# Kernel optimization log

Hardware: AMD Instinct MI355X
Metric: run time of the kernel (lower is better)

The kernel has to match this reference:

```python
import jax, jax.numpy as jnp
import numpy as np

B, N, D, H = 2, 256, 512, 8
DK = D // H


def _lin(x, w, b):
    # torch nn.Linear: y = x @ W.T + b, W is [out, in]
    return jnp.matmul(x, w.T) + b


def setup_inputs() -> dict:
    key = jax.random.key(0)
    ks = jax.random.split(key, 12)
    std = 0.02
    inp = {
        "x": jax.random.normal(ks[0], (B, N, D), jnp.float32),
        "batched_graphs": jax.random.normal(ks[1], (B, N, N, D), jnp.float32) * std,
        "mask": jnp.zeros((B, N, N), dtype=bool),
    }
    names = ["wq", "wk", "wv", "wo", "wl", "wr", "wrk", "wrv"]
    for i, n in enumerate(names):
        inp[n] = jax.random.normal(ks[2 + i], (D, D), jnp.float32) * std
        inp["b" + n[1:]] = jnp.zeros((D,), jnp.float32)
    return inp


def reference(x, batched_graphs, mask,
              wq, bq, wk, bk, wv, bv, wo, bo,
              wl, bl, wr, br, wrk, brk, wrv, brv):
    # update_relations: per-edge key/value maps
    graphs_k = _lin(batched_graphs, wrk, brk).reshape(B, N, N, H, DK)
    graphs_v = _lin(batched_graphs, wrv, brv).reshape(B, N, N, H, DK)

    query = _lin(x, wq, bq).reshape(B, N, H, DK)
    key_ = _lin(x, wk, bk).reshape(B, N, H, DK)
    value = _lin(x, wv, bv).reshape(B, N, H, DK)

    scores_k = jnp.einsum("bxhd,byhd->bxyh", query, key_)
    scores_g = jnp.einsum("bxhd,bxyhd->bxyh", query, graphs_k)
    scores = (scores_k + scores_g) / np.sqrt(DK).astype(np.float32)
    scores = jnp.where(mask[..., None], jnp.float32(-1e9), scores)
    p_attn = jax.nn.softmax(scores, axis=2)  # over key nodes y

    x_v = jnp.einsum("bxyh,byhd->bxhd", p_attn, value)
    x_g = jnp.einsum("bxyh,bxyhd->bxhd", p_attn, graphs_v)
    out = (x_v + x_g).reshape(B, N, D)

    # relation update: outer sum of left/right projections
    x_left = _lin(out, wl, bl)[:, :, None, :]   # [B,N,1,D]
    x_right = _lin(out, wr, br)[:, None, :, :]  # [B,1,N,D]
    new_graphs = x_left + x_right               # [B,N,N,D]

    return _lin(out, wo, bo), new_graphs
```

## Files before the change

### kernel.cpp

```cpp
#include <hip/hip_runtime.h>

#define BB 2
#define NN 256
#define DD 512
#define HH 8

typedef float f4raw __attribute__((ext_vector_type(4)));

__device__ __forceinline__ float dot4(float4 a, float4 b) {
    return a.x*b.x + a.y*b.y + a.z*b.z + a.w*b.w;
}

__device__ __forceinline__ float4 f4fma(float s, float4 a, float4 acc) {
    acc.x += s * a.x; acc.y += s * a.y; acc.z += s * a.z; acc.w += s * a.w;
    return acc;
}

__device__ __forceinline__ void gload_lds16(const void* g, void* l) {
    __builtin_amdgcn_global_load_lds(
        (const __attribute__((address_space(1))) unsigned int*)g,
        (__attribute__((address_space(3))) unsigned int*)l, 16, 0, 0);
}

__device__ __forceinline__ void stage_swz8(const char* rowbase, float4* dst, int w, int lane) {
    #pragma unroll
    for (int j = 0; j < 2; ++j) {
        const int f0 = w * 128 + j * 64;
        const int y = w;
        const int c = j * 64 + lane;
        gload_lds16(rowbase + (size_t)y * 2048 + ((size_t)(c ^ y) << 4), &dst[f0]);
    }
}

__global__ __launch_bounds__(64) void kProj(
    const float* __restrict__ in_,
    const float* __restrict__ w0, const float* __restrict__ b0,
    const float* __restrict__ w1, const float* __restrict__ b1,
    const float* __restrict__ w2, const float* __restrict__ b2,
    float* __restrict__ o0, float* __restrict__ o1, float* __restrict__ o2)
{
    __shared__ float4 xs[2][32 * 5];
    __shared__ float4 ws[2][32 * 5];

    const int t = threadIdx.x;
    const int blk = blockIdx.x;
    const int proj = blk >> 8;
    const int rem = blk & 255;
    const int row0 = (rem >> 4) * 32;
    const int col0 = (rem & 15) * 32;

    const float* W; const float* Bp; float* O;
    if (proj == 0)      { W = w0; Bp = b0; O = o0; }
    else if (proj == 1) { W = w1; Bp = b1; O = o1; }
    else                { W = w2; Bp = b2; O = o2; }

    const float4* X4 = (const float4*)in_ + (size_t)row0 * 128;
    const float4* W4 = (const float4*)W  + (size_t)col0 * 128;

    const int sr = t >> 2, se = t & 3;
    const int ty = t >> 3, tx = t & 7;

    float4 rx0 = X4[(size_t)sr * 128 + se];
    float4 rx1 = X4[(size_t)(sr + 16) * 128 + se];
    float4 rw0 = W4[(size_t)sr * 128 + se];
    float4 rw1 = W4[(size_t)(sr + 16) * 128 + se];
    xs[0][sr * 5 + se] = rx0;  xs[0][(sr + 16) * 5 + se] = rx1;
    ws[0][sr * 5 + se] = rw0;  ws[0][(sr + 16) * 5 + se] = rw1;

    float acc[4][4] = {};

    for (int q = 0; q < 32; ++q) {
        __syncthreads();
        const int cur = q & 1;
        if (q < 31) {
            const int ko = (q + 1) * 4;
            rx0 = X4[(size_t)sr * 128 + ko + se];
            rx1 = X4[(size_t)(sr + 16) * 128 + ko + se];
            rw0 = W4[(size_t)sr * 128 + ko + se];
            rw1 = W4[(size_t)(sr + 16) * 128 + ko + se];
        }
        const float4* xb = xs[cur];
        const float4* wb = ws[cur];
        #pragma unroll
        for (int e4 = 0; e4 < 4; ++e4) {
            float4 xr[4], wc[4];
            #pragma unroll
            for (int i = 0; i < 4; ++i) xr[i] = xb[(ty + 8 * i) * 5 + e4];
            #pragma unroll
            for (int j = 0; j < 4; ++j) wc[j] = wb[(tx + 8 * j) * 5 + e4];
            #pragma unroll
            for (int i = 0; i < 4; ++i)
                #pragma unroll
                for (int j = 0; j < 4; ++j)
                    acc[i][j] += dot4(xr[i], wc[j]);
        }
        if (q < 31) {
            const int nxt = cur ^ 1;
            xs[nxt][sr * 5 + se] = rx0;  xs[nxt][(sr + 16) * 5 + se] = rx1;
            ws[nxt][sr * 5 + se] = rw0;  ws[nxt][(sr + 16) * 5 + se] = rw1;
        }
    }

    float bb[4];
    #pragma unroll
    for (int j = 0; j < 4; ++j) bb[j] = Bp[col0 + tx + 8 * j];
    #pragma unroll
    for (int i = 0; i < 4; ++i) {
        const int orow = row0 + ty + 8 * i;
        #pragma unroll
        for (int j = 0; j < 4; ++j)
            O[(size_t)orow * DD + col0 + tx + 8 * j] = acc[i][j] + bb[j];
    }
}

__global__ __launch_bounds__(256) void kQkp(
    const float* __restrict__ q, const float* __restrict__ wrk,
    float* __restrict__ qkp)
{
    __shared__ float qs[8 * 64];
    const int t = threadIdx.x;
    const int blk = blockIdx.x;
    const int rowg = blk >> 5;
    const int h = (blk >> 2) & 7;
    const int eq = blk & 3;
    const int row0 = rowg * 8;
    {
        const int r = t >> 5, d2 = (t & 31) * 2;
        const float2 tmp = *(const float2*)(q + (size_t)(row0 + r) * DD + h * 64 + d2);
        qs[r * 64 + d2] = tmp.x; qs[r * 64 + d2 + 1] = tmp.y;
    }
    __syncthreads();
    const int e = eq * 128 + (t & 127);
    const int rp = (t >> 7) * 4;
    const float* wcol = wrk + (size_t)(h * 64) * DD + e;
    float a0 = 0, a1 = 0, a2 = 0, a3 = 0;
    #pragma unroll 8
    for (int d = 0; d < 64; ++d) {
        const float wv = wcol[(size_t)d * DD];
        a0 += qs[(rp + 0) * 64 + d] * wv;
        a1 += qs[(rp + 1) * 64 + d] * wv;
        a2 += qs[(rp + 2) * 64 + d] * wv;
        a3 += qs[(rp + 3) * 64 + d] * wv;
    }
    qkp[((size_t)(row0 + rp + 0) * HH + h) * DD + e] = a0;
    qkp[((size_t)(row0 + rp + 1) * HH + h) * DD + e] = a1;
    qkp[((size_t)(row0 + rp + 2) * HH + h) * DD + e] = a2;
    qkp[((size_t)(row0 + rp + 3) * HH + h) * DD + e] = a3;
}

__global__ __launch_bounds__(256) void kSk(
    const float* __restrict__ q, const float* __restrict__ k,
    const unsigned char* __restrict__ mask, float* __restrict__ sk)
{
    __shared__ float qs[8 * 65];
    __shared__ float ks[64 * 65];
    const int t = threadIdx.x;
    const int blk = blockIdx.x;
    const int b  = blk >> 10;
    const int h  = (blk >> 7) & 7;
    const int xt = (blk >> 2) & 31;
    const int yt = blk & 3;
    const int x0 = xt * 8, y0 = yt * 64;
    {
        const int r = t >> 5, d2 = (t & 31) * 2;
        const float2 tmp = *(const float2*)(q + (size_t)(b * NN + x0 + r) * DD + h * 64 + d2);
        qs[r * 65 + d2] = tmp.x; qs[r * 65 + d2 + 1] = tmp.y;
    }
    #pragma unroll
    for (int j = 0; j < 8; ++j) {
        const int f = t + 256 * j;
        const int r = f >> 5, d2 = (f & 31) * 2;
        const float2 tmp = *(const float2*)(k + (size_t)(b * NN + y0 + r) * DD + h * 64 + d2);
        ks[r * 65 + d2] = tmp.x; ks[r * 65 + d2 + 1] = tmp.y;
    }
    __syncthreads();
    const int xi = t >> 5, yg = t & 31;
    float a0 = 0, a1 = 0;
    #pragma unroll 8
    for (int d = 0; d < 64; ++d) {
        const float qv = qs[xi * 65 + d];
        a0 += qv * ks[(yg * 2 + 0) * 65 + d];
        a1 += qv * ks[(yg * 2 + 1) * 65 + d];
    }
    a0 *= 0.125f; a1 *= 0.125f;
    const unsigned char* mrow = mask + (size_t)(b * NN + x0 + xi) * NN;
    const int gy = y0 + yg * 2;
    if (mrow[gy + 0]) a0 = -1e9f;
    if (mrow[gy + 1]) a1 = -1e9f;
    float2 st; st.x = a0; st.y = a1;
    *(float2*)(sk + ((size_t)(b * NN + x0 + xi) * HH + h) * NN + gy) = st;
}

__global__ __launch_bounds__(512) void kC(
    const float* __restrict__ G, const float* __restrict__ sk,
    const float* __restrict__ qkp, const float* __restrict__ v,
    const float* __restrict__ wrv, const float* __restrict__ brv,
    float* __restrict__ om)
{
    __shared__ float4 gbuf[2][1024];
    __shared__ float4 qgc[1024];
    __shared__ float s_l[64];
    __shared__ float lL[8];
    __shared__ float xvs[512];

    const int t = threadIdx.x;
    const int lane = t & 63;
    const int w = t >> 6;
    const int bid = blockIdx.x;
    const int b = bid >> 8;

    const char* Grow = (const char*)(G + (size_t)bid * NN * DD);
    stage_swz8((const char*)(qkp + (size_t)bid * HH * DD), qgc, w, lane);
    stage_swz8(Grow, &gbuf[0][0], w, lane);

    const int s_  = t & 15;
    const int sg  = t >> 4;
    const int sy  = sg >> 2;
    const int h0i = (sg & 3) * 2;
    const int ec4 = t & 127;
    const int hb  = (t >> 7) * 2;
    const int hv  = t >> 6;
    const int dv  = t & 63;
    const int ri  = hv & 1;

    float4 gacc0 = {0,0,0,0}, gacc1 = {0,0,0,0};
    float m0 = -3e38f, m1 = -3e38f, l0 = 0, l1 = 0, vx = 0;

    const float* vcol = v + (size_t)(b * NN) * DD + hv * 64 + dv;
    const float* skrow = sk + (size_t)bid * HH * NN;

    __syncthreads();

    int cb = 0;
    for (int tt = 0; tt < 32; ++tt) {
        if (tt < 31)
            stage_swz8(Grow + (size_t)(tt + 1) * 8 * 2048, &gbuf[cb ^ 1][0], w, lane);

        float vvs[8];
        #pragma unroll
        for (int y = 0; y < 8; ++y) vvs[y] = vcol[((size_t)tt * 8 + y) * DD];

        {
            float a0 = 0, a1 = 0;
            const float4* gb = &gbuf[cb][0];
            #pragma unroll
            for (int i = 0; i < 8; ++i) {
                const int e4 = i * 16 + s_;
                const float4 g0 = gb[sy * 128 + (e4 ^ sy)];
                a0 += dot4(g0, qgc[h0i * 128 + (e4 ^ h0i)]);
                a1 += dot4(g0, qgc[(h0i + 1) * 128 + (e4 ^ (h0i + 1))]);
            }
            #pragma unroll
            for (int mm = 1; mm < 16; mm <<= 1) {
                a0 += __shfl_xor(a0, mm); a1 += __shfl_xor(a1, mm);
            }
            if (s_ < 2) {
                const float val = (s_ == 0) ? a0 : a1;
                const int h = h0i + s_;
                const int gy = tt * 8 + sy;
                s_l[sy * 8 + h] = val * 0.125f + skrow[(size_t)h * NN + gy];
            }
        }
        __syncthreads();

        float2 sv[8];
        #pragma unroll
        for (int y = 0; y < 8; ++y) sv[y] = *(const float2*)&s_l[y * 8 + hb];

        float mx0 = sv[0].x, mx1 = sv[0].y;
        #pragma unroll
        for (int y = 1; y < 8; ++y) {
            mx0 = fmaxf(mx0, sv[y].x); mx1 = fmaxf(mx1, sv[y].y);
        }
        const float n0 = fmaxf(m0, mx0), rs0 = __expf(m0 - n0);
        const float n1 = fmaxf(m1, mx1), rs1 = __expf(m1 - n1);
        m0 = n0; m1 = n1;
        l0 *= rs0; l1 *= rs1;
        gacc0.x *= rs0; gacc0.y *= rs0; gacc0.z *= rs0; gacc0.w *= rs0;
        gacc1.x *= rs1; gacc1.y *= rs1; gacc1.z *= rs1; gacc1.w *= rs1;
        vx *= ri ? rs1 : rs0;

        {
            const float4* gb = &gbuf[cb][0];
            #pragma unroll
            for (int y = 0; y < 8; ++y) {
                const float4 gv = gb[y * 128 + (ec4 ^ y)];
                const float p0 = __expf(sv[y].x - m0); l0 += p0; gacc0 = f4fma(p0, gv, gacc0);
                const float p1 = __expf(sv[y].y - m1); l1 += p1; gacc1 = f4fma(p1, gv, gacc1);
                vx += (ri ? p1 : p0) * vvs[y];
            }
        }
        __syncthreads();
        cb ^= 1;
    }

    qgc[(hb + 0) * 128 + ec4] = gacc0;
    qgc[(hb + 1) * 128 + ec4] = gacc1;
    if (ec4 == 0) { lL[hb] = l0; lL[hb + 1] = l1; }
    xvs[hv * 64 + dv] = vx;
    __syncthreads();

    #pragma unroll 2
    for (int oo = 0; oo < 16; ++oo) {
        const int o = sg * 16 + oo;
        const int ho = o >> 6;
        const float4* wr4 = (const float4*)(wrv + (size_t)o * DD);
        float acc = 0;
        #pragma unroll
        for (int i = 0; i < 8; ++i) {
            const int e4 = i * 16 + s_;
            acc += dot4(wr4[e4], qgc[ho * 128 + e4]);
        }
        #pragma unroll
        for (int mm = 1; mm < 16; mm <<= 1) acc += __shfl_xor(acc, mm);
        if (s_ == 0)
            om[(size_t)bid * DD + o] = (xvs[o] + acc) / lL[ho] + brv[o];
    }
}

__global__ __launch_bounds__(256) void kE(
    const float* __restrict__ xl, const float* __restrict__ xr,
    float* __restrict__ ng)
{
    const int t = threadIdx.x;
    const int blk = blockIdx.x;
    const int bid = blk >> 2;
    const int yc = blk & 3;
    const int b = bid >> 8;
    const int o4 = t & 127;
    const int yh = t >> 7;
    const float4 left = ((const float4*)xl)[(size_t)bid * 128 + o4];
    const float4* xr4 = (const float4*)xr + (size_t)b * NN * 128;
    f4raw* out4 = (f4raw*)ng + (size_t)bid * NN * 128;
    for (int y = yc * 64 + yh; y < yc * 64 + 64; y += 2) {
        const float4 rr = xr4[y * 128 + o4];
        f4raw s;
        s.x = left.x + rr.x; s.y = left.y + rr.y;
        s.z = left.z + rr.z; s.w = left.w + rr.w;
        __builtin_nontemporal_store(s, &out4[y * 128 + o4]);
    }
}

extern "C" void kernel_launch(void* const* d_in, const int* in_sizes, int n_in,
                              void* d_out, int out_size, void* d_ws, size_t ws_size,
                              hipStream_t stream)
{
    (void)in_sizes; (void)n_in; (void)out_size; (void)ws_size;
    const float* x    = (const float*)d_in[0];
    const float* G    = (const float*)d_in[1];
    const unsigned char* mask = (const unsigned char*)d_in[2];
    const float* wq  = (const float*)d_in[3];  const float* bq  = (const float*)d_in[4];
    const float* wk  = (const float*)d_in[5];  const float* bk  = (const float*)d_in[6];
    const float* wv  = (const float*)d_in[7];  const float* bv  = (const float*)d_in[8];
    const float* wo  = (const float*)d_in[9];  const float* bo  = (const float*)d_in[10];
    const float* wl  = (const float*)d_in[11]; const float* bl  = (const float*)d_in[12];
    const float* wr  = (const float*)d_in[13]; const float* br  = (const float*)d_in[14];
    const float* wrk = (const float*)d_in[15];
    const float* wrv = (const float*)d_in[17]; const float* brv = (const float*)d_in[18];

    float* out  = (float*)d_out;
    float* fout = out;
    float* ng   = out + (size_t)BB * NN * DD;

    const size_t ng_f  = (size_t)BB * NN * NN * DD;
    const size_t row_f = (size_t)BB * NN * DD;
    const size_t total = row_f * 17;
    float* base = ng + ng_f - total;
    float* q    = base;
    float* k    = q   + row_f;
    float* vv_  = k   + row_f;
    float* qkp  = vv_ + row_f;
    float* skp  = qkp + row_f * 8;
    float* om   = skp + row_f * 4;
    float* xl = (float*)d_ws;
    float* xr = xl + row_f;

    kProj<<<768, 64, 0, stream>>>(x, wq, bq, wk, bk, wv, bv, q, k, vv_);
    kQkp <<<2048, 256, 0, stream>>>(q, wrk, qkp);
    kSk  <<<2048, 256, 0, stream>>>(q, k, mask, skp);
    kC   <<<512, 512, 0, stream>>>(G, skp, qkp, vv_, wrv, brv, om);
    kProj<<<768, 64, 0, stream>>>(om, wo, bo, wl, bl, wr, br, fout, xl, xr);
    kE   <<<2048, 256, 0, stream>>>(xl, xr, ng);
}
```

Measured before the change: 305.7 us.

## Restructure edge-attention kernel into per-wave independent online softmax with split reduction

The main attention kernel moves from 512 to 256 threads. Each wave now owns two key rows per tile and keeps its own online-softmax state for all eight heads, so the per-tile block barriers go away and only explicit vmcnt waits gate the double-buffered global-to-LDS loads of G. The per-wave partial results are merged with a log-sum-exp combine and an LDS tree reduction. The value-side term is computed afterwards from stored scores instead of inside the loop. This trades more registers per thread and a serial 256-step value loop at the end for fewer synchronizations and better occupancy.

```diff
diff --git a/kernel.cpp b/kernel.cpp
--- a/kernel.cpp
+++ b/kernel.cpp
@@ -16,19 +16,36 @@
     return acc;
 }
 
+__device__ __forceinline__ float4 f4mul(float s, float4 a) {
+    a.x *= s; a.y *= s; a.z *= s; a.w *= s; return a;
+}
+
 __device__ __forceinline__ void gload_lds16(const void* g, void* l) {
     __builtin_amdgcn_global_load_lds(
         (const __attribute__((address_space(1))) unsigned int*)g,
         (__attribute__((address_space(3))) unsigned int*)l, 16, 0, 0);
 }
 
-__device__ __forceinline__ void stage_swz8(const char* rowbase, float4* dst, int w, int lane) {
-    #pragma unroll
-    for (int j = 0; j < 2; ++j) {
-        const int f0 = w * 128 + j * 64;
-        const int y = w;
-        const int c = j * 64 + lane;
+__device__ __forceinline__ void stage_swz(const char* rowbase, float4* dst, int w, int lane) {
+    #pragma unroll
+    for (int j = 0; j < 4; ++j) {
+        const int f0 = w * 256 + j * 64;
+        const int y = f0 >> 7;
+        const int c = (f0 & 127) + lane;
         gload_lds16(rowbase + (size_t)y * 2048 + ((size_t)(c ^ y) << 4), &dst[f0]);
+    }
+}
+
+__device__ __forceinline__ void stageG(const char* Grow, int tt, int w, int lane, float4* dst) {
+    #pragma unroll
+    for (int r = 0; r < 2; ++r) {
+        const int yr = 2 * w + r;
+        const char* src = Grow + (size_t)(tt * 8 + yr) * 2048;
+        #pragma unroll
+        for (int j = 0; j < 2; ++j) {
+            const int c = j * 64 + lane;
+            gload_lds16(src + ((size_t)(c ^ yr) << 4), &dst[r * 128 + j * 64]);
+        }
     }
 }
 
@@ -191,17 +208,17 @@
     *(float2*)(sk + ((size_t)(b * NN + x0 + xi) * HH + h) * NN + gy) = st;
 }
 
-__global__ __launch_bounds__(512) void kC(
+__global__ __launch_bounds__(256, 2) void kC(
     const float* __restrict__ G, const float* __restrict__ sk,
     const float* __restrict__ qkp, const float* __restrict__ v,
     const float* __restrict__ wrv, const float* __restrict__ brv,
     float* __restrict__ om)
 {
-    __shared__ float4 gbuf[2][1024];
-    __shared__ float4 qgc[1024];
-    __shared__ float s_l[64];
-    __shared__ float lL[8];
-    __shared__ float xvs[512];
+    __shared__ float4 Gdb[2][4][256];
+    __shared__ float4 qk4[1024];
+    __shared__ float  sk_l[2048];
+    __shared__ float  s_st[2048];
+    __shared__ float  ml[64];
 
     const int t = threadIdx.x;
     const int lane = t & 63;
@@ -210,111 +227,185 @@
     const int b = bid >> 8;
 
     const char* Grow = (const char*)(G + (size_t)bid * NN * DD);
-    stage_swz8((const char*)(qkp + (size_t)bid * HH * DD), qgc, w, lane);
-    stage_swz8(Grow, &gbuf[0][0], w, lane);
-
-    const int s_  = t & 15;
-    const int sg  = t >> 4;
-    const int sy  = sg >> 2;
-    const int h0i = (sg & 3) * 2;
-    const int ec4 = t & 127;
-    const int hb  = (t >> 7) * 2;
-    const int hv  = t >> 6;
-    const int dv  = t & 63;
-    const int ri  = hv & 1;
-
-    float4 gacc0 = {0,0,0,0}, gacc1 = {0,0,0,0};
-    float m0 = -3e38f, m1 = -3e38f, l0 = 0, l1 = 0, vx = 0;
-
-    const float* vcol = v + (size_t)(b * NN) * DD + hv * 64 + dv;
-    const float* skrow = sk + (size_t)bid * HH * NN;
-
-    __syncthreads();
+
+    stage_swz((const char*)(qkp + (size_t)bid * HH * DD), qk4, w, lane);
+    {
+        const char* skb = (const char*)(sk + (size_t)bid * HH * NN);
+        gload_lds16(skb + (size_t)(w * 128 + lane) * 16,      (float4*)sk_l + w * 128);
+        gload_lds16(skb + (size_t)(w * 128 + 64 + lane) * 16, (float4*)sk_l + w * 128 + 64);
+    }
+    stageG(Grow, 0, w, lane, &Gdb[0][w][0]);
+    asm volatile("s_waitcnt vmcnt(4)" ::: "memory");
+    __builtin_amdgcn_sched_barrier(0);
+    __builtin_amdgcn_s_barrier();
+
+    const int s_ = lane & 15;
+    const int g  = lane >> 4;
+    const int h0 = 2 * g;
+    const int yr0 = 2 * w, yr1 = 2 * w + 1;
+
+    float4 gA[8], gB[8];
+    float m[8], l[8];
+    #pragma unroll
+    for (int h = 0; h < 8; ++h) {
+        gA[h] = make_float4(0, 0, 0, 0); gB[h] = make_float4(0, 0, 0, 0);
+        m[h] = -3e38f; l[h] = 0.f;
+    }
 
     int cb = 0;
+    #pragma unroll 1
     for (int tt = 0; tt < 32; ++tt) {
-        if (tt < 31)
-            stage_swz8(Grow + (size_t)(tt + 1) * 8 * 2048, &gbuf[cb ^ 1][0], w, lane);
-
-        float vvs[8];
-        #pragma unroll
-        for (int y = 0; y < 8; ++y) vvs[y] = vcol[((size_t)tt * 8 + y) * DD];
+        __builtin_amdgcn_sched_barrier(0);
+        if (tt < 31) {
+            stageG(Grow, tt + 1, w, lane, &Gdb[cb ^ 1][w][0]);
+            asm volatile("s_waitcnt vmcnt(4)" ::: "memory");
+        } else {
+            asm volatile("s_waitcnt vmcnt(0)" ::: "memory");
+        }
+        __builtin_amdgcn_sched_barrier(0);
+
+        const float4* gb = &Gdb[cb][w][0];
+        const int gy0 = tt * 8 + yr0, gy1 = tt * 8 + yr1;
 
         {
-            float a0 = 0, a1 = 0;
-            const float4* gb = &gbuf[cb][0];
+            float a00 = 0, a01 = 0, a10 = 0, a11 = 0;
             #pragma unroll
             for (int i = 0; i < 8; ++i) {
                 const int e4 = i * 16 + s_;
-                const float4 g0 = gb[sy * 128 + (e4 ^ sy)];
-                a0 += dot4(g0, qgc[h0i * 128 + (e4 ^ h0i)]);
-                a1 += dot4(g0, qgc[(h0i + 1) * 128 + (e4 ^ (h0i + 1))]);
+                const float4 g0 = gb[(e4 ^ yr0)];
+                const float4 g1 = gb[128 + (e4 ^ yr1)];
+                const float4 p0 = qk4[h0 * 128 + (e4 ^ h0)];
+                const float4 p1 = qk4[(h0 + 1) * 128 + (e4 ^ (h0 + 1))];
+                a00 += dot4(g0, p0); a01 += dot4(g0, p1);
+                a10 += dot4(g1, p0); a11 += dot4(g1, p1);
             }
             #pragma unroll
             for (int mm = 1; mm < 16; mm <<= 1) {
-                a0 += __shfl_xor(a0, mm); a1 += __shfl_xor(a1, mm);
+                a00 += __shfl_xor(a00, mm); a01 += __shfl_xor(a01, mm);
+                a10 += __shfl_xor(a10, mm); a11 += __shfl_xor(a11, mm);
             }
-            if (s_ < 2) {
-                const float val = (s_ == 0) ? a0 : a1;
-                const int h = h0i + s_;
-                const int gy = tt * 8 + sy;
-                s_l[sy * 8 + h] = val * 0.125f + skrow[(size_t)h * NN + gy];
+            if (s_ < 4) {
+                const int yy = s_ & 1, hh = s_ >> 1;
+                const float val = yy ? (hh ? a11 : a10) : (hh ? a01 : a00);
+                const int h = h0 + hh;
+                const int gy = yy ? gy1 : gy0;
+                s_st[gy * 8 + h] = val * 0.125f + sk_l[h * 256 + gy];
             }
         }
-        __syncthreads();
-
-        float2 sv[8];
-        #pragma unroll
-        for (int y = 0; y < 8; ++y) sv[y] = *(const float2*)&s_l[y * 8 + hb];
-
-        float mx0 = sv[0].x, mx1 = sv[0].y;
-        #pragma unroll
-        for (int y = 1; y < 8; ++y) {
-            mx0 = fmaxf(mx0, sv[y].x); mx1 = fmaxf(mx1, sv[y].y);
-        }
-        const float n0 = fmaxf(m0, mx0), rs0 = __expf(m0 - n0);
-        const float n1 = fmaxf(m1, mx1), rs1 = __expf(m1 - n1);
-        m0 = n0; m1 = n1;
-        l0 *= rs0; l1 *= rs1;
-        gacc0.x *= rs0; gacc0.y *= rs0; gacc0.z *= rs0; gacc0.w *= rs0;
-        gacc1.x *= rs1; gacc1.y *= rs1; gacc1.z *= rs1; gacc1.w *= rs1;
-        vx *= ri ? rs1 : rs0;
-
-        {
-            const float4* gb = &gbuf[cb][0];
-            #pragma unroll
-            for (int y = 0; y < 8; ++y) {
-                const float4 gv = gb[y * 128 + (ec4 ^ y)];
-                const float p0 = __expf(sv[y].x - m0); l0 += p0; gacc0 = f4fma(p0, gv, gacc0);
-                const float p1 = __expf(sv[y].y - m1); l1 += p1; gacc1 = f4fma(p1, gv, gacc1);
-                vx += (ri ? p1 : p0) * vvs[y];
-            }
-        }
-        __syncthreads();
+
+        const float4 sva = *(const float4*)&s_st[gy0 * 8];
+        const float4 svb = *(const float4*)&s_st[gy0 * 8 + 4];
+        const float4 svc = *(const float4*)&s_st[gy1 * 8];
+        const float4 svd = *(const float4*)&s_st[gy1 * 8 + 4];
+        const float s0[8] = {sva.x, sva.y, sva.z, sva.w, svb.x, svb.y, svb.z, svb.w};
+        const float s1[8] = {svc.x, svc.y, svc.z, svc.w, svd.x, svd.y, svd.z, svd.w};
+
+        const float4 gr0a = gb[(lane ^ yr0)];
+        const float4 gr0b = gb[((lane + 64) ^ yr0)];
+        const float4 gr1a = gb[128 + (lane ^ yr1)];
+        const float4 gr1b = gb[128 + ((lane + 64) ^ yr1)];
+
+        #pragma unroll
+        for (int h = 0; h < 8; ++h) {
+            const float mn = fmaxf(m[h], fmaxf(s0[h], s1[h]));
+            const float rs = __expf(m[h] - mn);
+            const float p0 = __expf(s0[h] - mn);
+            const float p1 = __expf(s1[h] - mn);
+            m[h] = mn;
+            l[h] = l[h] * rs + p0 + p1;
+            gA[h] = f4fma(p1, gr1a, f4fma(p0, gr0a, f4mul(rs, gA[h])));
+            gB[h] = f4fma(p1, gr1b, f4fma(p0, gr0b, f4mul(rs, gB[h])));
+        }
         cb ^= 1;
     }
 
-    qgc[(hb + 0) * 128 + ec4] = gacc0;
-    qgc[(hb + 1) * 128 + ec4] = gacc1;
-    if (ec4 == 0) { lL[hb] = l0; lL[hb + 1] = l1; }
-    xvs[hv * 64 + dv] = vx;
-    __syncthreads();
-
-    #pragma unroll 2
-    for (int oo = 0; oo < 16; ++oo) {
-        const int o = sg * 16 + oo;
-        const int ho = o >> 6;
+    asm volatile("s_waitcnt vmcnt(0)" ::: "memory");
+    __syncthreads();
+    if (lane == 0) {
+        #pragma unroll
+        for (int h = 0; h < 8; ++h) { ml[w * 16 + h] = m[h]; ml[w * 16 + 8 + h] = l[h]; }
+    }
+    __syncthreads();
+
+    float M[8], Lf[8];
+    #pragma unroll
+    for (int h = 0; h < 8; ++h) {
+        const float m0 = ml[h], m1 = ml[16 + h], m2 = ml[32 + h], m3 = ml[48 + h];
+        const float mm = fmaxf(fmaxf(m0, m1), fmaxf(m2, m3));
+        M[h] = mm;
+        Lf[h] = __expf(m0 - mm) * ml[8 + h]  + __expf(m1 - mm) * ml[24 + h]
+              + __expf(m2 - mm) * ml[40 + h] + __expf(m3 - mm) * ml[56 + h];
+    }
+    #pragma unroll
+    for (int h = 0; h < 8; ++h) {
+        const float ws = __expf(m[h] - M[h]);
+        gA[h] = f4mul(ws, gA[h]); gB[h] = f4mul(ws, gB[h]);
+    }
+    float4* rA = &Gdb[0][0][0];
+    float4* rB = &Gdb[1][0][0];
+    if (w == 2) {
+        #pragma unroll
+        for (int h = 0; h < 8; ++h) { rA[h * 128 + lane] = gA[h]; rA[h * 128 + 64 + lane] = gB[h]; }
+    }
+    if (w == 3) {
+        #pragma unroll
+        for (int h = 0; h < 8; ++h) { rB[h * 128 + lane] = gA[h]; rB[h * 128 + 64 + lane] = gB[h]; }
+    }
+    __syncthreads();
+    if (w == 0) {
+        #pragma unroll
+        for (int h = 0; h < 8; ++h) {
+            gA[h].x += rA[h*128+lane].x; gA[h].y += rA[h*128+lane].y; gA[h].z += rA[h*128+lane].z; gA[h].w += rA[h*128+lane].w;
+            gB[h].x += rA[h*128+64+lane].x; gB[h].y += rA[h*128+64+lane].y; gB[h].z += rA[h*128+64+lane].z; gB[h].w += rA[h*128+64+lane].w;
+        }
+    }
+    if (w == 1) {
+        #pragma unroll
+        for (int h = 0; h < 8; ++h) {
+            gA[h].x += rB[h*128+lane].x; gA[h].y += rB[h*128+lane].y; gA[h].z += rB[h*128+lane].z; gA[h].w += rB[h*128+lane].w;
+            gB[h].x += rB[h*128+64+lane].x; gB[h].y += rB[h*128+64+lane].y; gB[h].z += rB[h*128+64+lane].z; gB[h].w += rB[h*128+64+lane].w;
+        }
+    }
+    __syncthreads();
+    if (w == 1) {
+        #pragma unroll
+        for (int h = 0; h < 8; ++h) { rA[h * 128 + lane] = gA[h]; rA[h * 128 + 64 + lane] = gB[h]; }
+    }
+    __syncthreads();
+    if (w == 0) {
+        #pragma unroll
+        for (int h = 0; h < 8; ++h) {
+            gA[h].x += rA[h*128+lane].x; gA[h].y += rA[h*128+lane].y; gA[h].z += rA[h*128+lane].z; gA[h].w += rA[h*128+lane].w;
+            gB[h].x += rA[h*128+64+lane].x; gB[h].y += rA[h*128+64+lane].y; gB[h].z += rA[h*128+64+lane].z; gB[h].w += rA[h*128+64+lane].w;
+            qk4[h * 128 + lane] = gA[h];
+            qk4[h * 128 + 64 + lane] = gB[h];
+        }
+    }
+    if (t == 0) {
+        #pragma unroll
+        for (int h = 0; h < 8; ++h) ml[h] = Lf[h];
+    }
+    {
+        #pragma unroll
+        for (int h = 0; h < 8; ++h) sk_l[t * 8 + h] = __expf(s_st[t * 8 + h] - M[h]);
+    }
+    __syncthreads();
+
+    const float* vb = v + (size_t)(b * NN) * DD;
+    #pragma unroll
+    for (int jj = 0; jj < 2; ++jj) {
+        const int o = jj * 256 + t;
+        const int h = o >> 6, d = o & 63;
         const float4* wr4 = (const float4*)(wrv + (size_t)o * DD);
+        const float4* gf = (const float4*)qk4 + h * 128;
         float acc = 0;
-        #pragma unroll
-        for (int i = 0; i < 8; ++i) {
-            const int e4 = i * 16 + s_;
-            acc += dot4(wr4[e4], qgc[ho * 128 + e4]);
-        }
-        #pragma unroll
-        for (int mm = 1; mm < 16; mm <<= 1) acc += __shfl_xor(acc, mm);
-        if (s_ == 0)
-            om[(size_t)bid * DD + o] = (xvs[o] + acc) / lL[ho] + brv[o];
+        #pragma unroll 4
+        for (int e4 = 0; e4 < 128; ++e4) acc += dot4(wr4[e4], gf[e4]);
+        float xv = 0;
+        const float* vc = vb + h * 64 + d;
+        #pragma unroll 4
+        for (int y = 0; y < 256; ++y) xv += sk_l[y * 8 + h] * vc[(size_t)y * DD];
+        om[(size_t)bid * DD + o] = (xv + acc) / ml[h] + brv[o];
     }
 }
 
@@ -364,7 +455,7 @@
 
     const size_t ng_f  = (size_t)BB * NN * NN * DD;
     const size_t row_f = (size_t)BB * NN * DD;
-    const size_t total = row_f * 17;
+    const size_t total = row_f * 16;
     float* base = ng + ng_f - total;
     float* q    = base;
     float* k    = q   + row_f;
@@ -378,7 +469,7 @@
     kProj<<<768, 64, 0, stream>>>(x, wq, bq, wk, bk, wv, bv, q, k, vv_);
     kQkp <<<2048, 256, 0, stream>>>(q, wrk, qkp);
     kSk  <<<2048, 256, 0, stream>>>(q, k, mask, skp);
-    kC   <<<512, 512, 0, stream>>>(G, skp, qkp, vv_, wrv, brv, om);
+    kC   <<<512, 256, 0, stream>>>(G, skp, qkp, vv_, wrv, brv, om);
     kProj<<<768, 64, 0, stream>>>(om, wo, bo, wl, bl, wr, br, fout, xl, xr);
     kE   <<<2048, 256, 0, stream>>>(xl, xr, ng);
 }
```

Measured after the change: 291.4 us. 1.05x faster.

## Split attention over key ranges into partial blocks with separate merge kernel

Applied to the files above, without the earlier changes.

The main attention kernel now splits each query row's 256 keys into four parts across 2048 blocks of 256 threads. Each block reads G directly into registers rather than staging it through LDS, and runs an online softmax per wave, merging the waves through LDS. Partial max, sum and accumulators go to scratch memory, and a new merge kernel combines them and applies the wrv projection. The aim is more parallelism and occupancy on the G stream, which dominates memory traffic, at the cost of an extra launch and partial-result traffic.

```diff
diff --git a/kernel.cpp b/kernel.cpp
--- a/kernel.cpp
+++ b/kernel.cpp
@@ -16,18 +16,22 @@
     return acc;
 }
 
+__device__ __forceinline__ float4 f4mul(float s, float4 a) {
+    a.x *= s; a.y *= s; a.z *= s; a.w *= s; return a;
+}
+
 __device__ __forceinline__ void gload_lds16(const void* g, void* l) {
     __builtin_amdgcn_global_load_lds(
         (const __attribute__((address_space(1))) unsigned int*)g,
         (__attribute__((address_space(3))) unsigned int*)l, 16, 0, 0);
 }
 
-__device__ __forceinline__ void stage_swz8(const char* rowbase, float4* dst, int w, int lane) {
-    #pragma unroll
-    for (int j = 0; j < 2; ++j) {
-        const int f0 = w * 128 + j * 64;
-        const int y = w;
-        const int c = j * 64 + lane;
+__device__ __forceinline__ void stage_swz(const char* rowbase, float4* dst, int w, int lane) {
+    #pragma unroll
+    for (int j = 0; j < 4; ++j) {
+        const int f0 = w * 256 + j * 64;
+        const int y = f0 >> 7;
+        const int c = (f0 & 127) + lane;
         gload_lds16(rowbase + (size_t)y * 2048 + ((size_t)(c ^ y) << 4), &dst[f0]);
     }
 }
@@ -191,131 +195,236 @@
     *(float2*)(sk + ((size_t)(b * NN + x0 + xi) * HH + h) * NN + gy) = st;
 }
 
-__global__ __launch_bounds__(512) void kC(
+__global__ __launch_bounds__(256, 3) void kC(
     const float* __restrict__ G, const float* __restrict__ sk,
     const float* __restrict__ qkp, const float* __restrict__ v,
+    float* __restrict__ pg, float* __restrict__ pxv,
+    float* __restrict__ pm, float* __restrict__ pl)
+{
+    __shared__ float4 qk4[1024];
+    __shared__ float4 mrg[1024];
+    __shared__ float4 xvm[128];
+    __shared__ float  ml[64];
+
+    const int t = threadIdx.x;
+    const int lane = t & 63;
+    const int w = t >> 6;
+    const int blk = blockIdx.x;
+    const int part = blk & 3;
+    const int bid = blk >> 2;
+    const int b = bid >> 8;
+    const int ybase = part * 64;
+
+    const int s_ = lane & 15;
+    const int g  = lane >> 4;
+    const int h0 = 2 * g, h1 = 2 * g + 1;
+    const int yr0 = 2 * w, yr1 = 2 * w + 1;
+
+    stage_swz((const char*)(qkp + (size_t)bid * HH * DD), qk4, w, lane);
+    asm volatile("s_waitcnt vmcnt(0)" ::: "memory");
+    __syncthreads();
+
+    float4 gagg0[8], gagg1[8];
+    #pragma unroll
+    for (int i = 0; i < 8; ++i) {
+        gagg0[i] = make_float4(0, 0, 0, 0);
+        gagg1[i] = make_float4(0, 0, 0, 0);
+    }
+    float4 xv0 = {0, 0, 0, 0}, xv1 = {0, 0, 0, 0};
+    float m0 = -3e38f, m1 = -3e38f, l0 = 0.f, l1 = 0.f;
+
+    const float4* Gb  = (const float4*)(G + (size_t)bid * NN * DD);
+    const float*  skb = sk + (size_t)bid * HH * NN;
+    const float4* vb4 = (const float4*)(v + (size_t)(b * NN) * DD);
+
+    #pragma unroll 1
+    for (int tt = 0; tt < 8; ++tt) {
+        const int gy0 = ybase + tt * 8 + yr0;
+        const int gy1 = gy0 + 1;
+
+        const float sk00 = skb[h0 * NN + gy0], sk01 = skb[h1 * NN + gy0];
+        const float sk10 = skb[h0 * NN + gy1], sk11 = skb[h1 * NN + gy1];
+        const float4 v00 = vb4[(size_t)gy0 * 128 + h0 * 16 + s_];
+        const float4 v01 = vb4[(size_t)gy0 * 128 + h1 * 16 + s_];
+        const float4 v10 = vb4[(size_t)gy1 * 128 + h0 * 16 + s_];
+        const float4 v11 = vb4[(size_t)gy1 * 128 + h1 * 16 + s_];
+
+        float4 g0[8], g1[8];
+        #pragma unroll
+        for (int i = 0; i < 8; ++i) g0[i] = Gb[(size_t)gy0 * 128 + i * 16 + s_];
+        #pragma unroll
+        for (int i = 0; i < 8; ++i) g1[i] = Gb[(size_t)gy1 * 128 + i * 16 + s_];
+
+        float a00 = 0, a01 = 0, a10 = 0, a11 = 0;
+        #pragma unroll
+        for (int i = 0; i < 8; ++i) {
+            const int e4 = i * 16 + s_;
+            const float4 q0 = qk4[h0 * 128 + (e4 ^ h0)];
+            const float4 q1 = qk4[h1 * 128 + (e4 ^ h1)];
+            a00 += dot4(g0[i], q0); a01 += dot4(g0[i], q1);
+            a10 += dot4(g1[i], q0); a11 += dot4(g1[i], q1);
+        }
+        #pragma unroll
+        for (int mm = 1; mm < 16; mm <<= 1) {
+            a00 += __shfl_xor(a00, mm); a01 += __shfl_xor(a01, mm);
+            a10 += __shfl_xor(a10, mm); a11 += __shfl_xor(a11, mm);
+        }
+        const float s00 = a00 * 0.125f + sk00;
+        const float s01 = a01 * 0.125f + sk01;
+        const float s10 = a10 * 0.125f + sk10;
+        const float s11 = a11 * 0.125f + sk11;
+
+        const float mn0 = fmaxf(m0, fmaxf(s00, s10));
+        const float rs0 = __expf(m0 - mn0);
+        const float p00 = __expf(s00 - mn0), p10 = __expf(s10 - mn0);
+        m0 = mn0; l0 = l0 * rs0 + p00 + p10;
+        const float mn1 = fmaxf(m1, fmaxf(s01, s11));
+        const float rs1 = __expf(m1 - mn1);
+        const float p01 = __expf(s01 - mn1), p11 = __expf(s11 - mn1);
+        m1 = mn1; l1 = l1 * rs1 + p01 + p11;
+
+        #pragma unroll
+        for (int i = 0; i < 8; ++i) {
+            gagg0[i] = f4fma(p10, g1[i], f4fma(p00, g0[i], f4mul(rs0, gagg0[i])));
+            gagg1[i] = f4fma(p11, g1[i], f4fma(p01, g0[i], f4mul(rs1, gagg1[i])));
+        }
+        xv0 = f4fma(p10, v10, f4fma(p00, v00, f4mul(rs0, xv0)));
+        xv1 = f4fma(p11, v11, f4fma(p01, v01, f4mul(rs1, xv1)));
+    }
+
+    if (s_ == 0) {
+        ml[w * 16 + h0] = m0;      ml[w * 16 + h1] = m1;
+        ml[w * 16 + 8 + h0] = l0;  ml[w * 16 + 8 + h1] = l1;
+    }
+    __syncthreads();
+    float M0, M1, L0, L1;
+    {
+        const float q0 = ml[h0], q1 = ml[16 + h0], q2 = ml[32 + h0], q3 = ml[48 + h0];
+        M0 = fmaxf(fmaxf(q0, q1), fmaxf(q2, q3));
+        L0 = __expf(q0 - M0) * ml[8 + h0]  + __expf(q1 - M0) * ml[24 + h0]
+           + __expf(q2 - M0) * ml[40 + h0] + __expf(q3 - M0) * ml[56 + h0];
+        const float r0 = ml[h1], r1 = ml[16 + h1], r2 = ml[32 + h1], r3 = ml[48 + h1];
+        M1 = fmaxf(fmaxf(r0, r1), fmaxf(r2, r3));
+        L1 = __expf(r0 - M1) * ml[8 + h1]  + __expf(r1 - M1) * ml[24 + h1]
+           + __expf(r2 - M1) * ml[40 + h1] + __expf(r3 - M1) * ml[56 + h1];
+    }
+    const float e0 = __expf(m0 - M0), e1 = __expf(m1 - M1);
+    #pragma unroll
+    for (int i = 0; i < 8; ++i) {
+        gagg0[i] = f4mul(e0, gagg0[i]);
+        gagg1[i] = f4mul(e1, gagg1[i]);
+    }
+    xv0 = f4mul(e0, xv0); xv1 = f4mul(e1, xv1);
+
+    #pragma unroll 1
+    for (int r = 3; r >= 1; --r) {
+        __syncthreads();
+        if (w == r) {
+            #pragma unroll
+            for (int i = 0; i < 8; ++i) {
+                mrg[h0 * 128 + i * 16 + s_] = gagg0[i];
+                mrg[h1 * 128 + i * 16 + s_] = gagg1[i];
+            }
+            xvm[h0 * 16 + s_] = xv0;
+            xvm[h1 * 16 + s_] = xv1;
+        }
+        __syncthreads();
+        if (w == r - 1) {
+            #pragma unroll
+            for (int i = 0; i < 8; ++i) {
+                const float4 u0 = mrg[h0 * 128 + i * 16 + s_];
+                const float4 u1 = mrg[h1 * 128 + i * 16 + s_];
+                gagg0[i].x += u0.x; gagg0[i].y += u0.y; gagg0[i].z += u0.z; gagg0[i].w += u0.w;
+                gagg1[i].x += u1.x; gagg1[i].y += u1.y; gagg1[i].z += u1.z; gagg1[i].w += u1.w;
+            }
+            const float4 xu0 = xvm[h0 * 16 + s_];
+            const float4 xu1 = xvm[h1 * 16 + s_];
+            xv0.x += xu0.x; xv0.y += xu0.y; xv0.z += xu0.z; xv0.w += xu0.w;
+            xv1.x += xu1.x; xv1.y += xu1.y; xv1.z += xu1.z; xv1.w += xu1.w;
+        }
+    }
+
+    if (w == 0) {
+        float4* pgb = (float4*)pg + (size_t)blk * 1024;
+        #pragma unroll
+        for (int i = 0; i < 8; ++i) {
+            pgb[h0 * 128 + i * 16 + s_] = gagg0[i];
+            pgb[h1 * 128 + i * 16 + s_] = gagg1[i];
+        }
+        float4* pxb = (float4*)pxv + (size_t)blk * 128;
+        pxb[h0 * 16 + s_] = xv0;
+        pxb[h1 * 16 + s_] = xv1;
+        if (s_ == 0) {
+            pm[blk * 8 + h0] = M0; pm[blk * 8 + h1] = M1;
+            pl[blk * 8 + h0] = L0; pl[blk * 8 + h1] = L1;
+        }
+    }
+}
+
+__global__ __launch_bounds__(256) void kM(
+    const float* __restrict__ pg, const float* __restrict__ pxv,
+    const float* __restrict__ pm, const float* __restrict__ pl,
     const float* __restrict__ wrv, const float* __restrict__ brv,
     float* __restrict__ om)
 {
-    __shared__ float4 gbuf[2][1024];
-    __shared__ float4 qgc[1024];
-    __shared__ float s_l[64];
-    __shared__ float lL[8];
-    __shared__ float xvs[512];
-
-    const int t = threadIdx.x;
-    const int lane = t & 63;
-    const int w = t >> 6;
-    const int bid = blockIdx.x;
-    const int b = bid >> 8;
-
-    const char* Grow = (const char*)(G + (size_t)bid * NN * DD);
-    stage_swz8((const char*)(qkp + (size_t)bid * HH * DD), qgc, w, lane);
-    stage_swz8(Grow, &gbuf[0][0], w, lane);
-
-    const int s_  = t & 15;
-    const int sg  = t >> 4;
-    const int sy  = sg >> 2;
-    const int h0i = (sg & 3) * 2;
-    const int ec4 = t & 127;
-    const int hb  = (t >> 7) * 2;
-    const int hv  = t >> 6;
-    const int dv  = t & 63;
-    const int ri  = hv & 1;
-
-    float4 gacc0 = {0,0,0,0}, gacc1 = {0,0,0,0};
-    float m0 = -3e38f, m1 = -3e38f, l0 = 0, l1 = 0, vx = 0;
-
-    const float* vcol = v + (size_t)(b * NN) * DD + hv * 64 + dv;
-    const float* skrow = sk + (size_t)bid * HH * NN;
-
-    __syncthreads();
-
-    int cb = 0;
-    for (int tt = 0; tt < 32; ++tt) {
-        if (tt < 31)
-            stage_swz8(Grow + (size_t)(tt + 1) * 8 * 2048, &gbuf[cb ^ 1][0], w, lane);
-
-        float vvs[8];
-        #pragma unroll
-        for (int y = 0; y < 8; ++y) vvs[y] = vcol[((size_t)tt * 8 + y) * DD];
-
-        {
-            float a0 = 0, a1 = 0;
-            const float4* gb = &gbuf[cb][0];
-            #pragma unroll
-            for (int i = 0; i < 8; ++i) {
-                const int e4 = i * 16 + s_;
-                const float4 g0 = gb[sy * 128 + (e4 ^ sy)];
-                a0 += dot4(g0, qgc[h0i * 128 + (e4 ^ h0i)]);
-                a1 += dot4(g0, qgc[(h0i + 1) * 128 + (e4 ^ (h0i + 1))]);
-            }
-            #pragma unroll
-            for (int mm = 1; mm < 16; mm <<= 1) {
-                a0 += __shfl_xor(a0, mm); a1 += __shfl_xor(a1, mm);
-            }
-            if (s_ < 2) {
-                const float val = (s_ == 0) ? a0 : a1;
-                const int h = h0i + s_;
-                const int gy = tt * 8 + sy;
-                s_l[sy * 8 + h] = val * 0.125f + skrow[(size_t)h * NN + gy];
-            }
-        }
-        __syncthreads();
-
-        float2 sv[8];
-        #pragma unroll
-        for (int y = 0; y < 8; ++y) sv[y] = *(const float2*)&s_l[y * 8 + hb];
-
-        float mx0 = sv[0].x, mx1 = sv[0].y;
-        #pragma unroll
-        for (int y = 1; y < 8; ++y) {
-            mx0 = fmaxf(mx0, sv[y].x); mx1 = fmaxf(mx1, sv[y].y);
-        }
-        const float n0 = fmaxf(m0, mx0), rs0 = __expf(m0 - n0);
-        const float n1 = fmaxf(m1, mx1), rs1 = __expf(m1 - n1);
-        m0 = n0; m1 = n1;
-        l0 *= rs0; l1 *= rs1;
-        gacc0.x *= rs0; gacc0.y *= rs0; gacc0.z *= rs0; gacc0.w *= rs0;
-        gacc1.x *= rs1; gacc1.y *= rs1; gacc1.z *= rs1; gacc1.w *= rs1;
-        vx *= ri ? rs1 : rs0;
-
-        {
-            const float4* gb = &gbuf[cb][0];
-            #pragma unroll
-            for (int y = 0; y < 8; ++y) {
-                const float4 gv = gb[y * 128 + (ec4 ^ y)];
-                const float p0 = __expf(sv[y].x - m0); l0 += p0; gacc0 = f4fma(p0, gv, gacc0);
-                const float p1 = __expf(sv[y].y - m1); l1 += p1; gacc1 = f4fma(p1, gv, gacc1);
-                vx += (ri ? p1 : p0) * vvs[y];
-            }
-        }
-        __syncthreads();
-        cb ^= 1;
-    }
-
-    qgc[(hb + 0) * 128 + ec4] = gacc0;
-    qgc[(hb + 1) * 128 + ec4] = gacc1;
-    if (ec4 == 0) { lL[hb] = l0; lL[hb + 1] = l1; }
-    xvs[hv * 64 + dv] = vx;
-    __syncthreads();
-
-    #pragma unroll 2
-    for (int oo = 0; oo < 16; ++oo) {
-        const int o = sg * 16 + oo;
-        const int ho = o >> 6;
-        const float4* wr4 = (const float4*)(wrv + (size_t)o * DD);
-        float acc = 0;
-        #pragma unroll
-        for (int i = 0; i < 8; ++i) {
-            const int e4 = i * 16 + s_;
-            acc += dot4(wr4[e4], qgc[ho * 128 + e4]);
-        }
-        #pragma unroll
-        for (int mm = 1; mm < 16; mm <<= 1) acc += __shfl_xor(acc, mm);
-        if (s_ == 0)
-            om[(size_t)bid * DD + o] = (xvs[o] + acc) / lL[ho] + brv[o];
-    }
+    __shared__ float4 gc[512];
+    __shared__ float xvs[256];
+    __shared__ float wexp[16], Ls[4];
+    const int t = threadIdx.x;
+    const int blk = blockIdx.x;
+    const int bid = blk >> 1;
+    const int half = blk & 1;
+    const int h0 = half * 4;
+    __shared__ float mlds[16], llds[16];
+    if (t < 16) {
+        const int i = t >> 2, hh = t & 3;
+        mlds[t] = pm[bid * 32 + i * 8 + h0 + hh];
+        llds[t] = pl[bid * 32 + i * 8 + h0 + hh];
+    }
+    __syncthreads();
+    if (t < 4) {
+        float M = mlds[t];
+        #pragma unroll
+        for (int i = 1; i < 4; ++i) M = fmaxf(M, mlds[i * 4 + t]);
+        float L = 0;
+        #pragma unroll
+        for (int i = 0; i < 4; ++i) {
+            const float wv = __expf(mlds[i * 4 + t] - M);
+            wexp[i * 4 + t] = wv;
+            L += wv * llds[i * 4 + t];
+        }
+        Ls[t] = L;
+    }
+    __syncthreads();
+    const int c4 = t & 127;
+    #pragma unroll
+    for (int r = 0; r < 2; ++r) {
+        const int hh = (t >> 7) * 2 + r;
+        float4 acc = {0, 0, 0, 0};
+        #pragma unroll
+        for (int i = 0; i < 4; ++i) {
+            const float wv = wexp[i * 4 + hh];
+            const float4 g = ((const float4*)pg)[((size_t)bid * 4 + i) * 1024 + (size_t)(h0 + hh) * 128 + c4];
+            acc.x += wv * g.x; acc.y += wv * g.y; acc.z += wv * g.z; acc.w += wv * g.w;
+        }
+        gc[hh * 128 + c4] = acc;
+    }
+    {
+        const int hh = t >> 6;
+        float s = 0;
+        #pragma unroll
+        for (int i = 0; i < 4; ++i)
+            s += wexp[i * 4 + hh] * pxv[((size_t)bid * 4 + i) * DD + half * 256 + t];
+        xvs[t] = s;
+    }
+    __syncthreads();
+    const int o = half * 256 + t;
+    const int hl = t >> 6;
+    const float4* wr4 = (const float4*)(wrv + (size_t)o * DD);
+    float acc = 0;
+    #pragma unroll 4
+    for (int e4 = 0; e4 < 128; ++e4) acc += dot4(wr4[e4], gc[hl * 128 + e4]);
+    om[(size_t)bid * DD + o] = (xvs[t] + acc) / Ls[hl] + brv[o];
 }
 
 __global__ __launch_bounds__(256) void kE(
@@ -364,21 +473,26 @@
 
     const size_t ng_f  = (size_t)BB * NN * NN * DD;
     const size_t row_f = (size_t)BB * NN * DD;
-    const size_t total = row_f * 17;
+    const size_t total = row_f * 52 + 32768;
     float* base = ng + ng_f - total;
     float* q    = base;
     float* k    = q   + row_f;
     float* vv_  = k   + row_f;
     float* qkp  = vv_ + row_f;
     float* skp  = qkp + row_f * 8;
-    float* om   = skp + row_f * 4;
+    float* pg   = skp + row_f * 4;
+    float* pxv  = pg  + row_f * 32;
+    float* pm   = pxv + row_f * 4;
+    float* pl   = pm  + 16384;
+    float* om   = pl  + 16384;
     float* xl = (float*)d_ws;
     float* xr = xl + row_f;
 
     kProj<<<768, 64, 0, stream>>>(x, wq, bq, wk, bk, wv, bv, q, k, vv_);
     kQkp <<<2048, 256, 0, stream>>>(q, wrk, qkp);
     kSk  <<<2048, 256, 0, stream>>>(q, k, mask, skp);
-    kC   <<<512, 512, 0, stream>>>(G, skp, qkp, vv_, wrv, brv, om);
+    kC   <<<2048, 256, 0, stream>>>(G, skp, qkp, vv_, pg, pxv, pm, pl);
+    kM   <<<1024, 256, 0, stream>>>(pg, pxv, pm, pl, wrv, brv, om);
     kProj<<<768, 64, 0, stream>>>(om, wo, bo, wl, bl, wr, br, fout, xl, xr);
     kE   <<<2048, 256, 0, stream>>>(xl, xr, ng);
 }
```

After: 740.1 us. 142% more time.
